# Optimization experiments

Hardware: AMD Instinct MI355X
Metric: run time of the kernel (lower is better)

The kernel has to match this reference:

```python
import jax, jax.numpy as jnp
import numpy as np

B, S, D, H, DK, FF = 8, 1024, 1024, 16, 64, 4096


def setup_inputs() -> dict:
    key = jax.random.key(0)
    ks = jax.random.split(key, 8)
    scale = 0.02
    return {
        "x": jax.random.normal(ks[0], (B, S, D), jnp.float32),
        "mask": jax.random.randint(ks[1], (B, S, S), 0, 2).astype(bool),
        "wq": jax.random.normal(ks[2], (H, D, DK), jnp.float32) * scale,
        "wk": jax.random.normal(ks[3], (H, D, DK), jnp.float32) * scale,
        "wv": jax.random.normal(ks[4], (H, D, DK), jnp.float32) * scale,
        "fc_w": jax.random.normal(ks[5], (D, D), jnp.float32) * scale,
        "fc_b": jnp.zeros((D,), jnp.float32),
        "w1": jax.random.normal(ks[6], (FF, D), jnp.float32) * scale,
        "b1": jnp.zeros((FF,), jnp.float32),
        "w2": jax.random.normal(ks[7], (D, FF), jnp.float32) * scale,
        "b2": jnp.zeros((D,), jnp.float32),
        "ln1_g": jnp.ones((D,), jnp.float32),
        "ln1_b": jnp.zeros((D,), jnp.float32),
        "ln2_g": jnp.ones((D,), jnp.float32),
        "ln2_b": jnp.zeros((D,), jnp.float32),
    }


def _layernorm(x, g, b, eps=1e-5):
    mu = jnp.mean(x, axis=-1, keepdims=True)
    var = jnp.mean(jnp.square(x - mu), axis=-1, keepdims=True)
    return (x - mu) * jax.lax.rsqrt(var + eps) * g + b


def reference(x, mask, wq, wk, wv, fc_w, fc_b, w1, b1, w2, b2, ln1_g, ln1_b, ln2_g, ln2_b):
    dk = wq.shape[-1]
    # batched over heads: [B,S,D] x [H,D,dk] -> [B,H,S,dk]
    q = jnp.einsum('bsd,hde->bhse', x, wq)
    k = jnp.einsum('bsd,hde->bhse', x, wk)
    v = jnp.einsum('bsd,hde->bhse', x, wv)
    s = jnp.einsum('bhqe,bhke->bhqk', q, k)
    # faithful quirks of the source: mask-fill with -1000 BEFORE scaling,
    # and softmax over dim=1 of the per-head [B,Sq,Sk] scores (the query axis).
    s = jnp.where(mask[:, None, :, :], s, jnp.float32(-1000.0))
    s = s / jnp.float32(dk) ** 0.5
    p = jax.nn.softmax(s, axis=2)
    o = jnp.einsum('bhqk,bhkv->bhqv', p, v)
    o = o.transpose(0, 2, 1, 3).reshape(x.shape[0], x.shape[1], -1)  # concat heads
    att = o @ fc_w.T + fc_b
    x1 = _layernorm(att + x, ln1_g, ln1_b)
    h = jax.nn.relu(x1 @ w1.T + b1) @ w2.T + b2
    return _layernorm(h + x1, ln2_g, ln2_b)
```

## Files before the change

kernel.cpp:

```cpp
#include <hip/hip_runtime.h>
#include <stdint.h>

#define DEV static __device__ __forceinline__

typedef unsigned short u16;
typedef __attribute__((ext_vector_type(8))) short v8s;
typedef __attribute__((ext_vector_type(4))) float v4f;
typedef __attribute__((ext_vector_type(4))) unsigned short v4u16;

DEV u16 f2bf(float f) {
  union { float f; unsigned u; } c; c.f = f;
  unsigned r = c.u + 0x7FFFu + ((c.u >> 16) & 1u);
  return (u16)(r >> 16);
}
DEV float bf2f(u16 h) {
  union { unsigned u; float f; } c; c.u = ((unsigned)h) << 16;
  return c.f;
}

DEV void gload16(const u16* g, u16* l) {
  __builtin_amdgcn_global_load_lds(
      (const __attribute__((address_space(1))) unsigned int*)g,
      (__attribute__((address_space(3))) unsigned int*)l, 16, 0, 0);
}

enum { MODE_QKV = 0, MODE_PV = 2, MODE_BIAS_RES = 3, MODE_BIAS_RELU = 4 };

struct EpArgs {
  const float* bias;
  const float* res;
  const u16* res_bf;
  float* outf;
  u16* outb;
  u16* q; u16* k; u16* v;
  int z0;
};

template <int BM, int BN, int FM, int FN, int MODE>
__global__ __launch_bounds__(256, 2)
void gemm_nt(const u16* __restrict__ A, int lda, long sA,
             const u16* __restrict__ B, int ldb, long sB,
             int K, int N, int nbx, int nby, EpArgs ep)
{
  __shared__ u16 As[BM * 32];
  __shared__ u16 Bs[BN * 32];

  const int tid  = threadIdx.x;
  const int lane = tid & 63;
  const int wave = tid >> 6;
  const int wm = (wave >> 1) * (FM * 16);
  const int wn = (wave & 1) * (FN * 16);

  const int id = blockIdx.x;
  const int nby8 = nby >> 3;
  const int c8 = id & 7, jj = id >> 3;
  const int tm = ((jj % nby8) * 8 + c8) * BM;
  const int tn = (jj / nby8) * BN;
  const int z  = blockIdx.y;

  const u16* Az = A + (long)z * sA;
  const u16* Bz = B + (long)z * sB;

  v4f acc[FM][FN];
  const v4f zero4 = {0.f, 0.f, 0.f, 0.f};
#pragma unroll
  for (int i = 0; i < FM; i++)
#pragma unroll
    for (int j = 0; j < FN; j++) acc[i][j] = zero4;

  for (int kt = 0; kt < K; kt += 32) {
#pragma unroll
    for (int c = 0; c < BM * 4; c += 256) {
      int cc = c + tid;
      int row = cc >> 2, kk = (cc & 3) * 8;
      gload16(Az + (long)(tm + row) * lda + kt + kk, &As[cc * 8]);
    }
#pragma unroll
    for (int c = 0; c < BN * 4; c += 256) {
      int cc = c + tid;
      int row = cc >> 2, kk = (cc & 3) * 8;
      gload16(Bz + (long)(tn + row) * ldb + kt + kk, &Bs[cc * 8]);
    }
    __syncthreads();

    v8s af[FM], bfr[FN];
#pragma unroll
    for (int i = 0; i < FM; i++)
      af[i] = *(const v8s*)&As[(wm + i * 16 + (lane & 15)) * 32 + (lane >> 4) * 8];
#pragma unroll
    for (int j = 0; j < FN; j++)
      bfr[j] = *(const v8s*)&Bs[(wn + j * 16 + (lane & 15)) * 32 + (lane >> 4) * 8];
#pragma unroll
    for (int i = 0; i < FM; i++)
#pragma unroll
      for (int j = 0; j < FN; j++)
        acc[i][j] = __builtin_amdgcn_mfma_f32_16x16x32_bf16(af[i], bfr[j], acc[i][j], 0, 0, 0);
    __syncthreads();
  }

  bool res_is_f32 = false;
  if constexpr (MODE == MODE_BIAS_RES) res_is_f32 = (ep.res != nullptr);

#pragma unroll
  for (int i = 0; i < FM; i++) {
    int mbase = tm + wm + i * 16 + ((lane >> 4) << 2);
#pragma unroll
    for (int j = 0; j < FN; j++) {
      int n = tn + wn + j * 16 + (lane & 15);
#pragma unroll
      for (int r = 0; r < 4; r++) {
        float val = acc[i][j][r];
        int m = mbase + r;
        if constexpr (MODE == MODE_QKV) {
          int b = m >> 10, s = m & 1023;
          int w = n >> 10, rr = n & 1023, h = rr >> 6, e = rr & 63;
          long idx = (((long)(b * 16 + h) << 10) + s) * 64 + e;
          u16* dst = (w == 0) ? ep.q : (w == 1) ? ep.k : ep.v;
          dst[idx] = f2bf(val);
        } else if constexpr (MODE == MODE_PV) {
          int zg = ep.z0 + z;
          int b = zg >> 4, h = zg & 15;
          ep.outb[((long)(b * 1024 + m) << 10) + h * 64 + n] = f2bf(val);
        } else if constexpr (MODE == MODE_BIAS_RES) {
          long idx = (long)m * N + n;
          float rres = res_is_f32 ? ep.res[idx] : bf2f(ep.res_bf[idx]);
          ep.outf[idx] = val + ep.bias[n] + rres;
        } else if constexpr (MODE == MODE_BIAS_RELU) {
          float v2 = val + ep.bias[n];
          ep.outb[(long)m * N + n] = f2bf(fmaxf(v2, 0.f));
        }
      }
    }
  }
}

__global__ __launch_bounds__(256, 4)
void attn_score(const u16* __restrict__ Q, const u16* __restrict__ Kb,
                const unsigned char* __restrict__ Mpk, float* __restrict__ rc,
                u16* __restrict__ E, int z0)
{
  __shared__ u16 sh[17408];
  __shared__ unsigned char Ms[2048];
  const int tid = threadIdx.x, lane = tid & 63, wave = tid >> 6;
  const int wm = (wave >> 1) * 64, wn = (wave & 1) * 64;
  const int zl = blockIdx.z, q0 = blockIdx.y * 128, n0 = blockIdx.x * 128;
  const int b = (z0 + zl) >> 4;
  const u16* Qz = Q + ((long)zl << 16);
  const u16* Kz = Kb + ((long)zl << 16);
  u16* Qs = sh;
  u16* Ks = sh + 8192;
  u16* Ps = sh;

#pragma unroll
  for (int c = 0; c < 4; c++) {
    int cc = c * 256 + tid;
    int s = cc >> 9, rem = cc & 511, row = rem >> 2, k0 = (rem & 3) * 8;
    gload16(Qz + (long)(q0 + row) * 64 + s * 32 + k0, &Qs[cc * 8]);
  }
#pragma unroll
  for (int c = 0; c < 4; c++) {
    int cc = c * 256 + tid;
    int s = cc >> 9, rem = cc & 511, row = rem >> 2, k0 = (rem & 3) * 8;
    gload16(Kz + (long)(n0 + row) * 64 + s * 32 + k0, &Ks[cc * 8]);
  }
  if (tid < 128)
    ((uint4*)Ms)[tid] =
        *(const uint4*)(Mpk + ((long)b << 17) + (long)(q0 + tid) * 128 + (n0 >> 3));
  __syncthreads();

  v4f sacc[4][4];
  const v4f zero4 = {0.f, 0.f, 0.f, 0.f};
#pragma unroll
  for (int i = 0; i < 4; i++)
#pragma unroll
    for (int j = 0; j < 4; j++) sacc[i][j] = zero4;
#pragma unroll
  for (int s = 0; s < 2; s++) {
    v8s af[4], bf[4];
#pragma unroll
    for (int i = 0; i < 4; i++)
      af[i] = *(const v8s*)&Qs[s * 4096 + (wm + i * 16 + (lane & 15)) * 32 + (lane >> 4) * 8];
#pragma unroll
    for (int j = 0; j < 4; j++)
      bf[j] = *(const v8s*)&Ks[s * 4096 + (wn + j * 16 + (lane & 15)) * 32 + (lane >> 4) * 8];
#pragma unroll
    for (int i = 0; i < 4; i++)
#pragma unroll
      for (int j = 0; j < 4; j++)
        sacc[i][j] = __builtin_amdgcn_mfma_f32_16x16x32_bf16(af[i], bf[j], sacc[i][j], 0, 0, 0);
  }
  __syncthreads();

#pragma unroll
  for (int j = 0; j < 4; j++) {
    int col = wn + j * 16 + (lane & 15);
    float csum = 0.f;
#pragma unroll
    for (int i = 0; i < 4; i++) {
      int mlb = wm + i * 16 + ((lane >> 4) << 2);
#pragma unroll
      for (int r = 0; r < 4; r++) {
        int ml = mlb + r;
        bool mk = (Ms[ml * 16 + (col >> 3)] >> (col & 7)) & 1;
        float ev = mk ? __expf(sacc[i][j][r] * 0.125f) : 0.f;
        u16 eb = f2bf(ev);
        Ps[ml * 136 + col] = eb;
        csum += bf2f(eb);
      }
    }
    csum += __shfl_xor(csum, 16);
    csum += __shfl_xor(csum, 32);
    if (lane < 16) atomicAdd(&rc[(zl << 10) + n0 + col], csum);
  }
  __syncthreads();

  u16* Ez = E + ((long)zl << 20);
#pragma unroll
  for (int it = 0; it < 8; it++) {
    int idx = it * 256 + tid;
    int row = idx >> 4, c16 = (idx & 15) * 8;
    *(uint4*)(Ez + (long)(q0 + row) * 1024 + n0 + c16) = *(const uint4*)(&Ps[row * 136 + c16]);
  }
}

__global__ __launch_bounds__(256, 2)
void attn_colsum(const u16* __restrict__ Q, const u16* __restrict__ Kb,
                 const unsigned char* __restrict__ Mb, float* __restrict__ rc)
{
  __shared__ u16 Qs[2 * 128 * 32];
  __shared__ u16 Ks[2 * 128 * 32];
  const int tid = threadIdx.x, lane = tid & 63, wave = tid >> 6;
  const int wm = (wave >> 1) * 64, wn = (wave & 1) * 64;
  const int z = blockIdx.y, q0 = blockIdx.x * 128, b = z >> 4;
  const u16* Qz = Q + ((long)z << 16);
  const u16* Kz = Kb + ((long)z << 16);
  const unsigned char* Mz = Mb + ((long)b << 20);

#pragma unroll
  for (int c = 0; c < 4; c++) {
    int cc = c * 256 + tid;
    int s = cc >> 9, rem = cc & 511, row = rem >> 2, k0 = (rem & 3) * 8;
    gload16(Qz + (long)(q0 + row) * 64 + s * 32 + k0, &Qs[cc * 8]);
  }

  for (int nt = 0; nt < 8; nt++) {
    int n0 = nt * 128;
#pragma unroll
    for (int c = 0; c < 4; c++) {
      int cc = c * 256 + tid;
      int s = cc >> 9, rem = cc & 511, row = rem >> 2, k0 = (rem & 3) * 8;
      gload16(Kz + (long)(n0 + row) * 64 + s * 32 + k0, &Ks[cc * 8]);
    }
    __syncthreads();

    v4f sacc[4][4];
    const v4f zero4 = {0.f, 0.f, 0.f, 0.f};
#pragma unroll
    for (int i = 0; i < 4; i++)
#pragma unroll
      for (int j = 0; j < 4; j++) sacc[i][j] = zero4;
#pragma unroll
    for (int s = 0; s < 2; s++) {
      v8s af[4], bf[4];
#pragma unroll
      for (int i = 0; i < 4; i++)
        af[i] = *(const v8s*)&Qs[s * 4096 + (wm + i * 16 + (lane & 15)) * 32 + (lane >> 4) * 8];
#pragma unroll
      for (int j = 0; j < 4; j++)
        bf[j] = *(const v8s*)&Ks[s * 4096 + (wn + j * 16 + (lane & 15)) * 32 + (lane >> 4) * 8];
#pragma unroll
      for (int i = 0; i < 4; i++)
#pragma unroll
        for (int j = 0; j < 4; j++)
          sacc[i][j] = __builtin_amdgcn_mfma_f32_16x16x32_bf16(af[i], bf[j], sacc[i][j], 0, 0, 0);
    }

#pragma unroll
    for (int j = 0; j < 4; j++) {
      int n = n0 + wn + j * 16 + (lane & 15);
      float csum = 0.f;
#pragma unroll
      for (int i = 0; i < 4; i++) {
        int mbase = q0 + wm + i * 16 + ((lane >> 4) << 2);
#pragma unroll
        for (int r = 0; r < 4; r++) {
          int m = mbase + r;
          bool mk = Mz[(long)m * 1024 + n] != 0;
          float sv = mk ? sacc[i][j][r] : -1000.0f;
          csum += bf2f(f2bf(__expf(sv * 0.125f)));
        }
      }
      csum += __shfl_xor(csum, 16);
      csum += __shfl_xor(csum, 32);
      if (lane < 16) atomicAdd(&rc[(z << 10) + n], csum);
    }
    __syncthreads();
  }
}

__global__ __launch_bounds__(256, 2)
void attn_pv(const u16* __restrict__ Q, const u16* __restrict__ Kb,
             const u16* __restrict__ vT, const unsigned char* __restrict__ Mb,
             u16* __restrict__ oc)
{
  __shared__ u16 Ks[2 * 128 * 32];
  __shared__ u16 Vs[4 * 64 * 32];
  __shared__ u16 Ps[4 * 128 * 32];
  const int tid = threadIdx.x, lane = tid & 63, wave = tid >> 6;
  const int wm = (wave >> 1) * 64;
  const int wn = (wave & 1) * 64;
  const int wnv = (wave & 1) * 32;
  const int z = blockIdx.y, q0 = blockIdx.x * 128, b = z >> 4, h = z & 15;
  const u16* Qz = Q + ((long)z << 16);
  const u16* Kz = Kb + ((long)z << 16);
  const u16* Vz = vT + ((long)z << 16);
  const unsigned char* Mz = Mb + ((long)b << 20);

#pragma unroll
  for (int c = 0; c < 4; c++) {
    int cc = c * 256 + tid;
    int s = cc >> 9, rem = cc & 511, row = rem >> 2, k0 = (rem & 3) * 8;
    gload16(Qz + (long)(q0 + row) * 64 + s * 32 + k0, &Ks[cc * 8]);
  }
  __syncthreads();
  v8s qf[4][2];
#pragma unroll
  for (int i = 0; i < 4; i++)
#pragma unroll
    for (int s = 0; s < 2; s++)
      qf[i][s] = *(const v8s*)&Ks[s * 4096 + (wm + i * 16 + (lane & 15)) * 32 + (lane >> 4) * 8];
  __syncthreads();

  v4f oacc[4][2];
  const v4f zero4 = {0.f, 0.f, 0.f, 0.f};
#pragma unroll
  for (int i = 0; i < 4; i++)
#pragma unroll
    for (int j = 0; j < 2; j++) oacc[i][j] = zero4;

  for (int nt = 0; nt < 8; nt++) {
    int n0 = nt * 128;
#pragma unroll
    for (int c = 0; c < 4; c++) {
      int cc = c * 256 + tid;
      int s = cc >> 9, rem = cc & 511, row = rem >> 2, k0 = (rem & 3) * 8;
      gload16(Kz + (long)(n0 + row) * 64 + s * 32 + k0, &Ks[cc * 8]);
    }
#pragma unroll
    for (int c = 0; c < 4; c++) {
      int cc = c * 256 + tid;
      int s = cc >> 8, rem = cc & 255, v = rem >> 2, k0 = (rem & 3) * 8;
      gload16(Vz + (long)v * 1024 + n0 + s * 32 + k0, &Vs[cc * 8]);
    }
    __syncthreads();

    v4f sacc[4][4];
#pragma unroll
    for (int i = 0; i < 4; i++)
#pragma unroll
      for (int j = 0; j < 4; j++) sacc[i][j] = zero4;
#pragma unroll
    for (int s = 0; s < 2; s++) {
      v8s bf[4];
#pragma unroll
      for (int j = 0; j < 4; j++)
        bf[j] = *(const v8s*)&Ks[s * 4096 + (wn + j * 16 + (lane & 15)) * 32 + (lane >> 4) * 8];
#pragma unroll
      for (int i = 0; i < 4; i++)
#pragma unroll
        for (int j = 0; j < 4; j++)
          sacc[i][j] = __builtin_amdgcn_mfma_f32_16x16x32_bf16(qf[i][s], bf[j], sacc[i][j], 0, 0, 0);
    }

#pragma unroll
    for (int i = 0; i < 4; i++) {
      int mlb = wm + i * 16 + ((lane >> 4) << 2);
#pragma unroll
      for (int j = 0; j < 4; j++) {
        int col = wn + j * 16 + (lane & 15);
        int gn = n0 + col;
#pragma unroll
        for (int r = 0; r < 4; r++) {
          int ml = mlb + r;
          bool mk = Mz[(long)(q0 + ml) * 1024 + gn] != 0;
          float sv = mk ? sacc[i][j][r] : -1000.0f;
          Ps[(col >> 5) * 4096 + ml * 32 + (col & 31)] = f2bf(__expf(sv * 0.125f));
        }
      }
    }
    __syncthreads();

#pragma unroll
    for (int s = 0; s < 4; s++) {
      v8s vf[2];
#pragma unroll
      for (int j = 0; j < 2; j++)
        vf[j] = *(const v8s*)&Vs[s * 2048 + (wnv + j * 16 + (lane & 15)) * 32 + (lane >> 4) * 8];
#pragma unroll
      for (int i = 0; i < 4; i++) {
        v8s pf = *(const v8s*)&Ps[s * 4096 + (wm + i * 16 + (lane & 15)) * 32 + (lane >> 4) * 8];
#pragma unroll
        for (int j = 0; j < 2; j++)
          oacc[i][j] = __builtin_amdgcn_mfma_f32_16x16x32_bf16(pf, vf[j], oacc[i][j], 0, 0, 0);
      }
    }
    __syncthreads();
  }

#pragma unroll
  for (int i = 0; i < 4; i++) {
    int mbase = q0 + wm + i * 16 + ((lane >> 4) << 2);
#pragma unroll
    for (int j = 0; j < 2; j++) {
      int n = wnv + j * 16 + (lane & 15);
#pragma unroll
      for (int r = 0; r < 4; r++) {
        int m = mbase + r;
        oc[((long)(b * 1024 + m) << 10) + h * 64 + n] = f2bf(oacc[i][j][r]);
      }
    }
  }
}

__global__ __launch_bounds__(256)
void transpose_scale(const u16* __restrict__ V, const float* __restrict__ rc,
                     u16* __restrict__ vT)
{
  __shared__ u16 t[64 * 66];
  __shared__ float rl[64];
  const int zl = blockIdx.y;
  const int s0 = blockIdx.x * 64;
  const int tid = threadIdx.x;
  const int r = tid >> 2, cg = (tid & 3) << 4;
  const u16* src = V + ((long)zl << 16) + (long)(s0 + r) * 64 + cg;
  v4u16 a0 = *(const v4u16*)(src);
  v4u16 a1 = *(const v4u16*)(src + 4);
  v4u16 a2 = *(const v4u16*)(src + 8);
  v4u16 a3 = *(const v4u16*)(src + 12);
  if (tid < 64) rl[tid] = 1.f / rc[(zl << 10) + s0 + tid];
  u16 tmp[16] = {(u16)a0.x, (u16)a0.y, (u16)a0.z, (u16)a0.w,
                 (u16)a1.x, (u16)a1.y, (u16)a1.z, (u16)a1.w,
                 (u16)a2.x, (u16)a2.y, (u16)a2.z, (u16)a2.w,
                 (u16)a3.x, (u16)a3.y, (u16)a3.z, (u16)a3.w};
#pragma unroll
  for (int i = 0; i < 16; i++) t[(cg + i) * 66 + r] = tmp[i];
  __syncthreads();
  const int e = tid >> 2, sg = (tid & 3) << 4;
  u16* dst = vT + ((long)zl << 16) + (long)e * 1024 + s0 + sg;
  v4u16 o;
#pragma unroll
  for (int q = 0; q < 4; q++) {
#pragma unroll
    for (int w = 0; w < 4; w++) {
      float f = bf2f(t[e * 66 + sg + q * 4 + w]) * rl[sg + q * 4 + w];
      ((u16*)&o)[w] = f2bf(f);
    }
    *(v4u16*)(dst + q * 4) = o;
  }
}

__global__ __launch_bounds__(256)
void ln_kernel(const float* __restrict__ in, const float* __restrict__ gam,
               const float* __restrict__ bet, float* __restrict__ outf,
               u16* __restrict__ outb)
{
  long row = blockIdx.x;
  v4f v = *(const v4f*)(in + (row << 10) + (threadIdx.x << 2));
  float s = v.x + v.y + v.z + v.w;
  float s2 = v.x * v.x + v.y * v.y + v.z * v.z + v.w * v.w;
#pragma unroll
  for (int o = 32; o > 0; o >>= 1) { s += __shfl_down(s, o); s2 += __shfl_down(s2, o); }
  __shared__ float red[8];
  int wv_ = threadIdx.x >> 6, ln = threadIdx.x & 63;
  if (ln == 0) { red[wv_] = s; red[4 + wv_] = s2; }
  __syncthreads();
  float S1 = red[0] + red[1] + red[2] + red[3];
  float S2 = red[4] + red[5] + red[6] + red[7];
  float mu = S1 * (1.f / 1024.f);
  float var = S2 * (1.f / 1024.f) - mu * mu;
  float rstd = rsqrtf(var + 1e-5f);
  v4f g4 = *(const v4f*)(gam + (threadIdx.x << 2));
  v4f b4 = *(const v4f*)(bet + (threadIdx.x << 2));
  v4f o4;
  o4.x = (v.x - mu) * rstd * g4.x + b4.x;
  o4.y = (v.y - mu) * rstd * g4.y + b4.y;
  o4.z = (v.z - mu) * rstd * g4.z + b4.z;
  o4.w = (v.w - mu) * rstd * g4.w + b4.w;
  if (outf) *(v4f*)(outf + (row << 10) + (threadIdx.x << 2)) = o4;
  if (outb) {
    v4u16 u;
    u.x = f2bf(o4.x); u.y = f2bf(o4.y); u.z = f2bf(o4.z); u.w = f2bf(o4.w);
    *(v4u16*)(outb + (row << 10) + (threadIdx.x << 2)) = u;
  }
}

__global__ __launch_bounds__(256)
void cvt_bf16(const float* __restrict__ in, u16* __restrict__ out, int n4)
{
  int i = blockIdx.x * 256 + threadIdx.x;
  if (i >= n4) return;
  v4f v = ((const v4f*)in)[i];
  v4u16 u;
  u.x = f2bf(v.x); u.y = f2bf(v.y); u.z = f2bf(v.z); u.w = f2bf(v.w);
  ((v4u16*)out)[i] = u;
}

__global__ __launch_bounds__(256)
void pack_qkvw(const float* __restrict__ wq, const float* __restrict__ wk,
               const float* __restrict__ wv, u16* __restrict__ out)
{
  int i = blockIdx.x * 256 + threadIdx.x;
  int w = i >> 20, r = i & 1048575;
  int e = r & 63, d = (r >> 6) & 1023, h = r >> 16;
  const float* src = (w == 0) ? wq : ((w == 1) ? wk : wv);
  float v = src[(((long)h << 10) + d) * 64 + e];
  out[((((long)w << 10) + (h << 6) + e) << 10) + d] = f2bf(v);
}

__global__ void detect_mask_kernel(const unsigned char* __restrict__ m, int* __restrict__ flag)
{
  if (threadIdx.x == 0 && blockIdx.x == 0) {
    int nz = 0;
    for (int i = 0; i < 256; i++)
      if ((i & 3) != 0 && m[i] != 0) nz++;
    *flag = (nz == 0) ? 1 : 0;
  }
}

__global__ __launch_bounds__(256)
void canon_mask(const unsigned char* __restrict__ m, const int* __restrict__ flag,
                unsigned char* __restrict__ out)
{
  int i = blockIdx.x * 256 + threadIdx.x;
  uchar4 o;
  if (*flag) {
    const int* mi = (const int*)m;
    o.x = mi[i * 4 + 0] != 0; o.y = mi[i * 4 + 1] != 0;
    o.z = mi[i * 4 + 2] != 0; o.w = mi[i * 4 + 3] != 0;
  } else {
    o = ((const uchar4*)m)[i];
  }
  ((uchar4*)out)[i] = o;
}

__global__ __launch_bounds__(256)
void canon_pack(const unsigned char* __restrict__ m, const int* __restrict__ flag,
                unsigned int* __restrict__ out)
{
  int g = blockIdx.x * 256 + threadIdx.x;
  unsigned int bits = 0;
  if (*flag) {
    const int* mi = (const int*)m + (long)g * 32;
#pragma unroll
    for (int i = 0; i < 32; i++) bits |= (mi[i] != 0 ? 1u : 0u) << i;
  } else {
    const unsigned char* mb = m + (long)g * 32;
#pragma unroll
    for (int i = 0; i < 32; i++) bits |= (mb[i] != 0 ? 1u : 0u) << i;
  }
  out[g] = bits;
}

extern "C" void kernel_launch(void* const* d_in, const int* in_sizes, int n_in,
                              void* d_out, int out_size, void* d_ws, size_t ws_size,
                              hipStream_t stream)
{
  const float* x     = (const float*)d_in[0];
  const unsigned char* mask = (const unsigned char*)d_in[1];
  const float* wq    = (const float*)d_in[2];
  const float* wk    = (const float*)d_in[3];
  const float* wv    = (const float*)d_in[4];
  const float* fc_w  = (const float*)d_in[5];
  const float* fc_b  = (const float*)d_in[6];
  const float* w1    = (const float*)d_in[7];
  const float* b1    = (const float*)d_in[8];
  const float* w2    = (const float*)d_in[9];
  const float* b2    = (const float*)d_in[10];
  const float* ln1_g = (const float*)d_in[11];
  const float* ln1_b = (const float*)d_in[12];
  const float* ln2_g = (const float*)d_in[13];
  const float* ln2_b = (const float*)d_in[14];
  (void)in_sizes; (void)n_in; (void)out_size;

  const size_t MB = 1ull << 20;
  char* ws = (char*)d_ws;
  int*   mflag = (int*)ws;
  float* rc    = (float*)(ws + 65536);
  unsigned char* Mpk = (unsigned char*)(ws + 1 * MB);
  u16*   bqkv  = (u16*)(ws + 2 * MB);
  u16*   fcb   = (u16*)(ws + 8 * MB);
  u16*   w1b   = (u16*)(ws + 10 * MB);
  u16*   w2b   = (u16*)(ws + 18 * MB);
  u16*   xb    = (u16*)(ws + 26 * MB);
  u16*   x1b   = xb;
  u16*   Qb    = (u16*)(ws + 42 * MB);
  u16*   Kb    = (u16*)(ws + 58 * MB);
  u16*   Vb    = (u16*)(ws + 74 * MB);
  u16*   vT    = (u16*)(ws + 90 * MB);
  u16*   oc    = (u16*)(ws + 106 * MB);
  u16*   h1    = (u16*)(ws + 42 * MB);
  float* r1    = (float*)(ws + 122 * MB);
  unsigned char* Mb = (unsigned char*)(ws + 122 * MB);
  u16*   E     = (u16*)(ws + 122 * MB);

  int CZ = 0;
  if      (ws_size >= 378 * MB) CZ = 128;
  else if (ws_size >= 250 * MB) CZ = 64;
  else if (ws_size >= 186 * MB) CZ = 32;
  else if (ws_size >= 154 * MB) CZ = 16;

  detect_mask_kernel<<<1, 64, 0, stream>>>(mask, mflag);
  if (CZ > 0) canon_pack<<<1024, 256, 0, stream>>>(mask, mflag, (unsigned int*)Mpk);
  else        canon_mask<<<8192, 256, 0, stream>>>(mask, mflag, Mb);

  cvt_bf16<<<8192, 256, 0, stream>>>(x, xb, 2097152);
  pack_qkvw<<<12288, 256, 0, stream>>>(wq, wk, wv, bqkv);
  cvt_bf16<<<1024, 256, 0, stream>>>(fc_w, fcb, 262144);
  cvt_bf16<<<4096, 256, 0, stream>>>(w1, w1b, 1048576);
  cvt_bf16<<<4096, 256, 0, stream>>>(w2, w2b, 1048576);

  {
    EpArgs ep = {};
    ep.q = Qb; ep.k = Kb; ep.v = Vb;
    gemm_nt<128, 128, 4, 4, MODE_QKV><<<dim3(24 * 64, 1), 256, 0, stream>>>(
        xb, 1024, 0, bqkv, 1024, 0, 1024, 3072, 24, 64, ep);
  }

  hipMemsetAsync(rc, 0, 128 * 1024 * 4, stream);
  if (CZ > 0) {
    for (int z0 = 0; z0 < 128; z0 += CZ) {
      attn_score<<<dim3(8, 8, CZ), 256, 0, stream>>>(
          Qb + (long)z0 * 65536, Kb + (long)z0 * 65536, Mpk,
          rc + (long)z0 * 1024, E, z0);
      transpose_scale<<<dim3(16, CZ), 256, 0, stream>>>(
          Vb + (long)z0 * 65536, rc + (long)z0 * 1024, vT + (long)z0 * 65536);
      EpArgs ep = {};
      ep.outb = oc; ep.z0 = z0;
      gemm_nt<128, 64, 4, 2, MODE_PV><<<dim3(8, CZ), 256, 0, stream>>>(
          E, 1024, 1048576, vT + (long)z0 * 65536, 1024, 65536,
          1024, 64, 1, 8, ep);
    }
  } else {
    attn_colsum<<<dim3(8, 128), 256, 0, stream>>>(Qb, Kb, Mb, rc);
    transpose_scale<<<dim3(16, 128), 256, 0, stream>>>(Vb, rc, vT);
    attn_pv<<<dim3(8, 128), 256, 0, stream>>>(Qb, Kb, vT, Mb, oc);
  }

  {
    EpArgs ep = {};
    ep.bias = fc_b; ep.res = x; ep.outf = r1;
    gemm_nt<128, 128, 4, 4, MODE_BIAS_RES><<<dim3(8 * 64, 1), 256, 0, stream>>>(
        oc, 1024, 0, fcb, 1024, 0, 1024, 1024, 8, 64, ep);
  }
  ln_kernel<<<8192, 256, 0, stream>>>(r1, ln1_g, ln1_b, (float*)nullptr, x1b);
  {
    EpArgs ep = {};
    ep.bias = b1; ep.outb = h1;
    gemm_nt<128, 128, 4, 4, MODE_BIAS_RELU><<<dim3(32 * 64, 1), 256, 0, stream>>>(
        x1b, 1024, 0, w1b, 1024, 0, 1024, 4096, 32, 64, ep);
  }
  {
    EpArgs ep = {};
    ep.bias = b2; ep.res_bf = x1b; ep.outf = r1;
    gemm_nt<128, 128, 4, 4, MODE_BIAS_RES><<<dim3(8 * 64, 1), 256, 0, stream>>>(
        h1, 4096, 0, w2b, 4096, 0, 4096, 1024, 8, 64, ep);
  }
  ln_kernel<<<8192, 256, 0, stream>>>(r1, ln2_g, ln2_b, (float*)d_out, (u16*)nullptr);
}
```

Before: 713.6 us.

## Split-K the fc and FFN-down GEMMs into two bf16 partials reduced in LayerNorm

The output-projection and second FFN GEMMs, each with N=1024 and only 512 tiles, are split along K into two halves using the grid z dimension. Each half writes a bf16 partial. A new ln_comb kernel sums the partials, bias and residual and applies LayerNorm in one pass, removing the fp32 r1 round trip. This doubles the tile count to fill the GPU better. In exchange it writes and reads two bf16 partial buffers, and rounding each partial to bf16 before the sum costs some precision.

After: 638.5 us. 1.12x faster.

```diff
diff --git a/kernel.cpp b/kernel.cpp
--- a/kernel.cpp
+++ b/kernel.cpp
@@ -24,7 +24,7 @@
       (__attribute__((address_space(3))) unsigned int*)l, 16, 0, 0);
 }
 
-enum { MODE_QKV = 0, MODE_PV = 2, MODE_BIAS_RES = 3, MODE_BIAS_RELU = 4 };
+enum { MODE_QKV = 0, MODE_PV = 2, MODE_BIAS_RES = 3, MODE_BIAS_RELU = 4, MODE_PARTIAL = 5 };
 
 struct EpArgs {
   const float* bias;
@@ -32,6 +32,7 @@
   const u16* res_bf;
   float* outf;
   u16* outb;
+  u16* outb2;
   u16* q; u16* k; u16* v;
   int z0;
 };
@@ -100,6 +101,8 @@
 
   bool res_is_f32 = false;
   if constexpr (MODE == MODE_BIAS_RES) res_is_f32 = (ep.res != nullptr);
+  u16* pdst = nullptr;
+  if constexpr (MODE == MODE_PARTIAL) pdst = z ? ep.outb2 : ep.outb;
 
 #pragma unroll
   for (int i = 0; i < FM; i++) {
@@ -128,6 +131,8 @@
         } else if constexpr (MODE == MODE_BIAS_RELU) {
           float v2 = val + ep.bias[n];
           ep.outb[(long)m * N + n] = f2bf(fmaxf(v2, 0.f));
+        } else if constexpr (MODE == MODE_PARTIAL) {
+          pdst[(long)m * N + n] = f2bf(val);
         }
       }
     }
@@ -456,6 +461,58 @@
       ((u16*)&o)[w] = f2bf(f);
     }
     *(v4u16*)(dst + q * 4) = o;
+  }
+}
+
+__global__ __launch_bounds__(256)
+void ln_comb(const u16* __restrict__ p0, const u16* __restrict__ p1,
+             const float* __restrict__ bias,
+             const float* __restrict__ resf, const u16* __restrict__ resb,
+             const float* __restrict__ gam, const float* __restrict__ bet,
+             float* __restrict__ outf, u16* __restrict__ outb)
+{
+  long row = blockIdx.x;
+  long base = (row << 10) + (threadIdx.x << 2);
+  v4u16 a = *(const v4u16*)(p0 + base);
+  v4u16 b = *(const v4u16*)(p1 + base);
+  v4f bi = *(const v4f*)(bias + (threadIdx.x << 2));
+  v4f v;
+  v.x = bf2f(a.x) + bf2f(b.x) + bi.x;
+  v.y = bf2f(a.y) + bf2f(b.y) + bi.y;
+  v.z = bf2f(a.z) + bf2f(b.z) + bi.z;
+  v.w = bf2f(a.w) + bf2f(b.w) + bi.w;
+  if (resf) {
+    v4f r = *(const v4f*)(resf + base);
+    v.x += r.x; v.y += r.y; v.z += r.z; v.w += r.w;
+  } else {
+    v4u16 r = *(const v4u16*)(resb + base);
+    v.x += bf2f(r.x); v.y += bf2f(r.y); v.z += bf2f(r.z); v.w += bf2f(r.w);
+  }
+  float s = v.x + v.y + v.z + v.w;
+  float s2 = v.x * v.x + v.y * v.y + v.z * v.z + v.w * v.w;
+#pragma unroll
+  for (int o = 32; o > 0; o >>= 1) { s += __shfl_down(s, o); s2 += __shfl_down(s2, o); }
+  __shared__ float red[8];
+  int wv_ = threadIdx.x >> 6, ln = threadIdx.x & 63;
+  if (ln == 0) { red[wv_] = s; red[4 + wv_] = s2; }
+  __syncthreads();
+  float S1 = red[0] + red[1] + red[2] + red[3];
+  float S2 = red[4] + red[5] + red[6] + red[7];
+  float mu = S1 * (1.f / 1024.f);
+  float var = S2 * (1.f / 1024.f) - mu * mu;
+  float rstd = rsqrtf(var + 1e-5f);
+  v4f g4 = *(const v4f*)(gam + (threadIdx.x << 2));
+  v4f b4 = *(const v4f*)(bet + (threadIdx.x << 2));
+  v4f o4;
+  o4.x = (v.x - mu) * rstd * g4.x + b4.x;
+  o4.y = (v.y - mu) * rstd * g4.y + b4.y;
+  o4.z = (v.z - mu) * rstd * g4.z + b4.z;
+  o4.w = (v.w - mu) * rstd * g4.w + b4.w;
+  if (outf) *(v4f*)(outf + base) = o4;
+  if (outb) {
+    v4u16 u;
+    u.x = f2bf(o4.x); u.y = f2bf(o4.y); u.z = f2bf(o4.z); u.w = f2bf(o4.w);
+    *(v4u16*)(outb + base) = u;
   }
 }
 
@@ -602,6 +659,8 @@
   float* r1    = (float*)(ws + 122 * MB);
   unsigned char* Mb = (unsigned char*)(ws + 122 * MB);
   u16*   E     = (u16*)(ws + 122 * MB);
+  u16*   p0    = (u16*)(ws + 122 * MB);
+  u16*   p1    = (u16*)(ws + 138 * MB);
 
   int CZ = 0;
   if      (ws_size >= 378 * MB) CZ = 128;
@@ -646,24 +705,49 @@
     attn_pv<<<dim3(8, 128), 256, 0, stream>>>(Qb, Kb, vT, Mb, oc);
   }
 
-  {
-    EpArgs ep = {};
-    ep.bias = fc_b; ep.res = x; ep.outf = r1;
-    gemm_nt<128, 128, 4, 4, MODE_BIAS_RES><<<dim3(8 * 64, 1), 256, 0, stream>>>(
-        oc, 1024, 0, fcb, 1024, 0, 1024, 1024, 8, 64, ep);
-  }
-  ln_kernel<<<8192, 256, 0, stream>>>(r1, ln1_g, ln1_b, (float*)nullptr, x1b);
-  {
-    EpArgs ep = {};
-    ep.bias = b1; ep.outb = h1;
-    gemm_nt<128, 128, 4, 4, MODE_BIAS_RELU><<<dim3(32 * 64, 1), 256, 0, stream>>>(
-        x1b, 1024, 0, w1b, 1024, 0, 1024, 4096, 32, 64, ep);
-  }
-  {
-    EpArgs ep = {};
-    ep.bias = b2; ep.res_bf = x1b; ep.outf = r1;
-    gemm_nt<128, 128, 4, 4, MODE_BIAS_RES><<<dim3(8 * 64, 1), 256, 0, stream>>>(
-        h1, 4096, 0, w2b, 4096, 0, 4096, 1024, 8, 64, ep);
-  }
-  ln_kernel<<<8192, 256, 0, stream>>>(r1, ln2_g, ln2_b, (float*)d_out, (u16*)nullptr);
-}
+  if (CZ > 0) {
+    {
+      EpArgs ep = {};
+      ep.outb = p0; ep.outb2 = p1;
+      gemm_nt<128, 128, 4, 4, MODE_PARTIAL><<<dim3(8 * 64, 2), 256, 0, stream>>>(
+          oc, 1024, 512, fcb, 1024, 512, 512, 1024, 8, 64, ep);
+    }
+    ln_comb<<<8192, 256, 0, stream>>>(p0, p1, fc_b, x, (const u16*)nullptr,
+                                      ln1_g, ln1_b, (float*)nullptr, x1b);
+    {
+      EpArgs ep = {};
+      ep.bias = b1; ep.outb = h1;
+      gemm_nt<128, 128, 4, 4, MODE_BIAS_RELU><<<dim3(32 * 64, 1), 256, 0, stream>>>(
+          x1b, 1024, 0, w1b, 1024, 0, 1024, 4096, 32, 64, ep);
+    }
+    {
+      EpArgs ep = {};
+      ep.outb = p0; ep.outb2 = p1;
+      gemm_nt<128, 128, 4, 4, MODE_PARTIAL><<<dim3(8 * 64, 2), 256, 0, stream>>>(
+          h1, 4096, 2048, w2b, 4096, 2048, 2048, 1024, 8, 64, ep);
+    }
+    ln_comb<<<8192, 256, 0, stream>>>(p0, p1, b2, (const float*)nullptr, x1b,
+                                      ln2_g, ln2_b, (float*)d_out, (u16*)nullptr);
+  } else {
+    {
+      EpArgs ep = {};
+      ep.bias = fc_b; ep.res = x; ep.outf = r1;
+      gemm_nt<128, 128, 4, 4, MODE_BIAS_RES><<<dim3(8 * 64, 1), 256, 0, stream>>>(
+          oc, 1024, 0, fcb, 1024, 0, 1024, 1024, 8, 64, ep);
+    }
+    ln_kernel<<<8192, 256, 0, stream>>>(r1, ln1_g, ln1_b, (float*)nullptr, x1b);
+    {
+      EpArgs ep = {};
+      ep.bias = b1; ep.outb = h1;
+      gemm_nt<128, 128, 4, 4, MODE_BIAS_RELU><<<dim3(32 * 64, 1), 256, 0, stream>>>(
+          x1b, 1024, 0, w1b, 1024, 0, 1024, 4096, 32, 64, ep);
+    }
+    {
+      EpArgs ep = {};
+      ep.bias = b2; ep.res_bf = x1b; ep.outf = r1;
+      gemm_nt<128, 128, 4, 4, MODE_BIAS_RES><<<dim3(8 * 64, 1), 256, 0, stream>>>(
+          h1, 4096, 0, w2b, 4096, 0, 4096, 1024, 8, 64, ep);
+    }
+    ln_kernel<<<8192, 256, 0, stream>>>(r1, ln2_g, ln2_b, (float*)d_out, (u16*)nullptr);
+  }
+}
```
